# Performance work log

Hardware: AMD Instinct MI355X
Metric: run time of the kernel (lower is better)

Reference implementation:

```python
import math
import jax, jax.numpy as jnp
import numpy as np

# ---- static hyperparams (match init_kwargs) ----
B, D, K, NC, F = 16384, 64, 128, 64, 256
TAU_MIN = 0.01
TAU_DENOM_MIN = 0.001
EPS = 0.001  # transport_eps


def setup_inputs() -> dict:
    key = jax.random.key(0)
    ks = jax.random.split(key, 8)
    # latent positions strictly inside the Poincare ball (norm < 0.9)
    z = jax.random.normal(ks[0], (B, D), jnp.float32)
    z = z / (jnp.linalg.norm(z, axis=-1, keepdims=True) + 1e-6)
    z = z * (0.9 * jax.random.uniform(ks[1], (B, 1), jnp.float32))
    features = jax.random.normal(ks[2], (B, F), jnp.float32)
    q_z_w = jax.random.normal(ks[3], (K, D), jnp.float32) * 0.02
    q_z_b = jnp.zeros((K,), jnp.float32)
    q_feat_w = jax.random.normal(ks[4], (K, F), jnp.float32) * 0.02
    q_feat_b = jnp.zeros((K,), jnp.float32)
    q_gamma = jax.random.normal(ks[5], (K, D, D), jnp.float32) * 0.02
    chart_queries = jax.random.normal(ks[6], (NC, K), jnp.float32) * 0.02
    return {"z": z, "features": features, "q_z_w": q_z_w, "q_z_b": q_z_b,
            "q_feat_w": q_feat_w, "q_feat_b": q_feat_b, "q_gamma": q_gamma,
            "chart_queries": chart_queries}


def _hyperbolic_score(z, centers):
    # z: [B, D]; centers: [NC, D] -> scores [B, NC]
    diff = z[:, None, :] - centers[None, :, :]
    dist_sq = (diff ** 2).sum(-1)                       # [B, NC]
    z_sq = (z ** 2).sum(-1, keepdims=True)              # [B, 1]
    c_sq = (centers ** 2).sum(-1)[None, :]              # [1, NC]
    denom = (1.0 - z_sq) * (1.0 - c_sq)
    arg = 1.0 + 2.0 * dist_sq / (denom + EPS)
    dist = jnp.arccosh(jnp.maximum(arg, 1.0 + EPS))
    # metric-aware temperature tau(z)
    tau = math.sqrt(K) * jnp.maximum(1.0 - z_sq[:, 0], TAU_DENOM_MIN) / 2.0
    tau = jnp.maximum(tau, TAU_MIN)                     # [B]
    return -dist / tau[:, None]


def reference(z, features, q_z_w, q_z_b, q_feat_w, q_feat_b, q_gamma, chart_queries):
    # chart centers live in the first D coords of the chart queries
    centers = chart_queries[:, :D]                      # [NC, D]
    scores = _hyperbolic_score(z, centers)              # [B, NC]

    # query: linear(z) + linear(features) + bilinear gamma term
    q = z @ q_z_w.T + q_z_b + features @ q_feat_w.T + q_feat_b   # [B, K]
    q = q + jnp.einsum("bi,bj,kij->bk", z, z, q_gamma)           # gamma contraction

    # O(n) hyperbolic parallel transport: scale queries by 1/lambda(z)
    r2 = jnp.minimum((z ** 2).sum(-1, keepdims=True), 1.0 - EPS)  # [B, 1]
    lam = 2.0 / (1.0 - r2 + EPS)                                  # [B, 1]
    tq = chart_queries[None, :, :] / lam[:, None, :]              # [B, NC, K]

    scores = scores + jnp.einsum("bk,bnk->bn", q, tq) / math.sqrt(K)
    weights = jax.nn.softmax(scores, axis=-1)           # [B, NC] (soft routing)
    k_chart = jnp.argmax(weights, axis=-1)              # [B]
    return weights, k_chart
```

## Files before the change

### kernel.cpp

```cpp
#include <hip/hip_runtime.h>
#include <hip/hip_bf16.h>
#include <cmath>
#include <cstring>

#define B_TOT 16384

typedef unsigned int uint_t;
typedef unsigned short ushort_t;
typedef __attribute__((ext_vector_type(8))) short bf16x8;
typedef __attribute__((ext_vector_type(16))) float f32x16;

#define WS_TAB 0
#define WS_CSQ 1024
#define WS_LIN 4096
#define WS_S   4198400
#define WS_PPK 5246976

__global__ __launch_bounds__(256) void prep_s(const float* __restrict__ g,
                                              const float* __restrict__ cq,
                                              char* __restrict__ ws) {
  __shared__ float gl[128][68];
  __shared__ float cql[16][132];
  float* S = (float*)(ws + WS_S);
  const int ns = blockIdx.x >> 6, J = blockIdx.x & 63, t = threadIdx.x;
  for (int i = t; i < 2048; i += 256) {
    const int k = i >> 4, c4 = (i & 15) * 4;
    *(float4*)&gl[k][c4] = *(const float4*)(g + (size_t)k * 4096 + J * 64 + c4);
  }
  for (int i = t; i < 2048; i += 256) {
    const int n16 = i >> 7, k = i & 127;
    cql[n16][k] = cq[(ns * 16 + n16) * 128 + k];
  }
  __syncthreads();
  const int n16 = t >> 4, c4 = (t & 15) * 4;
  float4 acc = {0.f, 0.f, 0.f, 0.f};
#pragma unroll 8
  for (int k = 0; k < 128; ++k) {
    const float w = cql[n16][k];
    const float4 gv = *(const float4*)&gl[k][c4];
    acc.x = fmaf(w, gv.x, acc.x);
    acc.y = fmaf(w, gv.y, acc.y);
    acc.z = fmaf(w, gv.z, acc.z);
    acc.w = fmaf(w, gv.w, acc.w);
  }
  *(float4*)(S + (size_t)(ns * 16 + n16) * 4096 + J * 64 + c4) = acc;
}

__global__ __launch_bounds__(256) void prep_pack(
    const float* __restrict__ qfw, const float* __restrict__ cq,
    const float* __restrict__ qzw, const float* __restrict__ qzb,
    const float* __restrict__ qfb, char* __restrict__ ws) {
  __shared__ float Sl[4096];
  __shared__ uint_t tabl[192];
  __shared__ float psumf[128][2];
  const int n = blockIdx.x & 63, part = blockIdx.x >> 6, t = threadIdx.x;
  const float* __restrict__ S = (const float*)(ws + WS_S) + (size_t)n * 4096;
  for (int i = t; i < 4096; i += 256) Sl[i] = S[i];
  if (t < 64) {
    const int i = t;
    const int start = (i < 16) ? 4 * i
                     : (i < 32) ? 64 + 3 * (i - 16)
                     : (i < 48) ? 112 + 2 * (i - 32)
                                : 144 + (i - 48);
    const int nst = 4 - (i >> 4);
    for (int u = 0; u < nst; ++u)
      tabl[start + u] = (0u << 16) | ((uint_t)i << 8) | (uint_t)(16 * ((i >> 4) + u));
  } else if (t < 80) tabl[160 + (t - 64)] = (1u << 16) | (uint_t)((t - 64) * 16);
  else if (t < 84)   tabl[176 + (t - 80)] = (2u << 16) | (uint_t)((t - 80) * 16);
  else if (t == 84)  tabl[180] = (3u << 16);
  else if (t < 96)   tabl[181 + (t - 85)] = 0;
  __syncthreads();
  if (part == 0 && n == 0 && t < 192) ((uint_t*)(ws + WS_TAB))[t] = tabl[t];

  const int mt = n >> 5, r = n & 31;
  auto wpack = [&](int s, int jo, float val) {
    const __hip_bfloat16 hb = __float2bfloat16(val);
    const float hf = __bfloat162float(hb);
    const __hip_bfloat16 lb = __float2bfloat16(val - hf);
    ushort_t hu, lu;
    memcpy(&hu, &hb, 2);
    memcpy(&lu, &lb, 2);
    const size_t base =
        (((size_t)s * 4 + mt * 2) * 64 + ((jo >> 3) & 1) * 32 + r) * 16 + (jo & 7) * 2;
    *(ushort_t*)(ws + WS_PPK + base) = hu;
    *(ushort_t*)(ws + WS_PPK + base + 1024) = lu;
  };

  for (int v = part * 640 + t; v < (part + 1) * 640; v += 256) {
    const int s = v >> 4, jo = v & 15;
    const uint_t inf = tabl[s];
    const int i = (inf >> 8) & 255, j0 = inf & 255;
    const int j = j0 + jo;
    const float val =
        (j < i) ? 0.f : ((j > i) ? Sl[i * 64 + j] + Sl[j * 64 + i] : Sl[i * 64 + i]);
    wpack(s, jo, val);
  }
  const float* __restrict__ cqn = cq + n * 128;

  if (part >= 2) {
    const int fl = t & 127, kh = t >> 7;
    const int f = (part - 2) * 128 + fl;
    float a = 0.f;
#pragma unroll 8
    for (int k = 0; k < 64; ++k)
      a = fmaf(qfw[(kh * 64 + k) * 256 + f], cqn[kh * 64 + k], a);
    psumf[fl][kh] = a;
    __syncthreads();
    if (t < 128) {
      const int ff = (part - 2) * 128 + t;
      wpack(160 + (ff >> 4), ff & 15, psumf[t][0] + psumf[t][1]);
    }
  } else if (part == 1) {
    if (t < 64) {
      float a = 0.f;
#pragma unroll 8
      for (int k = 0; k < 128; ++k) a = fmaf(cqn[k], qzw[k * 64 + t], a);
      wpack(176 + (t >> 4), t & 15, a);
    }
    for (int v2 = t; v2 < 176; v2 += 256) wpack(181 + (v2 >> 4), v2 & 15, 0.f);
  } else {
    if (t == 128) {
      float a = 0.f;
      for (int k = 0; k < 128; ++k) a = fmaf(qzb[k] + qfb[k], cqn[k], a);
      wpack(180, 0, a);
    } else if (t > 128 && t < 144) wpack(180, t - 128, 0.f);
    if (t == 144) {
      double a = 0.0;
      for (int d = 0; d < 64; ++d) a = fma((double)cqn[d], (double)cqn[d], a);
      ((double*)(ws + WS_CSQ))[n] = a;
    }
  }
}

__global__ __launch_bounds__(256, 4) void gemm_tail_kernel(
    const float* __restrict__ z, const float* __restrict__ feat,
    const float* __restrict__ cq, char* __restrict__ ws,
    float* __restrict__ out) {
  __shared__ __align__(16) unsigned char smem[46208];
  float (*z_lds)[68] = (float (*)[68])(smem);
  float (*s_lin)[65] = (float (*)[65])(smem + 8704);
  float (*zt)[33] = (float (*)[33])(smem + 17024);
  float (*cqT)[65] = (float (*)[65])(smem + 25472);
  double (*s_exp)[65] = (double (*)[65])(smem + 25472);
  double (*pmax)[9] = (double (*)[9])(smem + 42112);
  int (*parg)[9] = (int (*)[9])(smem + 44416);
  double* rowmax = (double*)(smem + 45568);
  int* rowarg = (int*)(smem + 45824);
  double* rowinv = (double*)(smem + 45952);

  const int t = threadIdx.x, lane = t & 63;
  const int wv = __builtin_amdgcn_readfirstlane(t >> 6);
  const int b0 = blockIdx.x * 32;
  const int h = lane >> 5, c = lane & 31;

  for (int i = t; i < 2048; i += 256) z_lds[i >> 6][i & 63] = z[(size_t)b0 * 64 + i];
  if (t < 128) z_lds[t >> 2][64 + (t & 3)] = 0.f;
  for (int i = t; i < 32 * 65; i += 256) ((float*)s_lin)[i] = 0.f;
  __syncthreads();

  const bf16x8* __restrict__ pp = (const bf16x8*)(ws + WS_PPK);
  f32x16 acc[2] = {};
#pragma unroll 2
  for (int it = 0; it < 46; ++it) {
    const int s = wv + it * 4;
    int mode, i_idx, p0;
    if (s < 64) {
      mode = 0; i_idx = s >> 2; p0 = (s & 3) * 16;
    } else if (s < 112) {
      const int q = s - 64, d = (q * 86) >> 8;
      mode = 0; i_idx = 16 + d; p0 = (q - 3 * d + 1) * 16;
    } else if (s < 144) {
      const int q = s - 112;
      mode = 0; i_idx = 32 + (q >> 1); p0 = ((q & 1) + 2) * 16;
    } else if (s < 160) {
      mode = 0; i_idx = s - 96; p0 = 48;
    } else if (s < 176) {
      mode = 1; i_idx = 0; p0 = (s - 160) * 16;
    } else if (s < 180) {
      mode = 2; i_idx = 0; p0 = (s - 176) * 16;
    } else {
      mode = 3; i_idx = 0; p0 = 0;
    }
    const bf16x8 Ah0 = pp[((size_t)s * 4 + 0) * 64 + lane];
    const bf16x8 Al0 = pp[((size_t)s * 4 + 1) * 64 + lane];
    const bf16x8 Ah1 = pp[((size_t)s * 4 + 2) * 64 + lane];
    const bf16x8 Al1 = pp[((size_t)s * 4 + 3) * 64 + lane];
    const int bl = c;
    float xv[8];
    if (mode == 0) {
      const float zi = z_lds[bl][i_idx];
      const float* __restrict__ zp = &z_lds[bl][p0 + h * 8];
      const float4 a = *(const float4*)zp, b2 = *(const float4*)(zp + 4);
      xv[0] = zi * a.x; xv[1] = zi * a.y; xv[2] = zi * a.z; xv[3] = zi * a.w;
      xv[4] = zi * b2.x; xv[5] = zi * b2.y; xv[6] = zi * b2.z; xv[7] = zi * b2.w;
    } else if (mode == 1) {
      const float* __restrict__ fp = feat + (size_t)(b0 + bl) * 256 + p0 + h * 8;
      const float4 a = *(const float4*)fp, b2 = *(const float4*)(fp + 4);
      xv[0] = a.x; xv[1] = a.y; xv[2] = a.z; xv[3] = a.w;
      xv[4] = b2.x; xv[5] = b2.y; xv[6] = b2.z; xv[7] = b2.w;
    } else if (mode == 2) {
      const float* __restrict__ zp = &z_lds[bl][p0 + h * 8];
      const float4 a = *(const float4*)zp, b2 = *(const float4*)(zp + 4);
      xv[0] = a.x; xv[1] = a.y; xv[2] = a.z; xv[3] = a.w;
      xv[4] = b2.x; xv[5] = b2.y; xv[6] = b2.z; xv[7] = b2.w;
    } else {
      xv[0] = (h == 0) ? 1.f : 0.f;
      xv[1] = xv[2] = xv[3] = xv[4] = xv[5] = xv[6] = xv[7] = 0.f;
    }
    uint_t bhw[4], blw[4];
#pragma unroll
    for (int e2 = 0; e2 < 4; ++e2) {
      const float2 xp = {xv[2 * e2], xv[2 * e2 + 1]};
      const __hip_bfloat162 hb2 = __float22bfloat162_rn(xp);
      uint_t hw;
      memcpy(&hw, &hb2, 4);
      const float h0 = __uint_as_float(hw << 16);
      const float h1 = __uint_as_float(hw & 0xffff0000u);
      const float2 lp = {xp.x - h0, xp.y - h1};
      const __hip_bfloat162 lb2 = __float22bfloat162_rn(lp);
      uint_t lw;
      memcpy(&lw, &lb2, 4);
      bhw[e2] = hw;
      blw[e2] = lw;
    }
    bf16x8 Bh, Bl;
    memcpy(&Bh, bhw, 16);
    memcpy(&Bl, blw, 16);
    acc[0] = __builtin_amdgcn_mfma_f32_32x32x16_bf16(Ah0, Bh, acc[0], 0, 0, 0);
    acc[0] = __builtin_amdgcn_mfma_f32_32x32x16_bf16(Ah0, Bl, acc[0], 0, 0, 0);
    acc[0] = __builtin_amdgcn_mfma_f32_32x32x16_bf16(Al0, Bh, acc[0], 0, 0, 0);
    acc[1] = __builtin_amdgcn_mfma_f32_32x32x16_bf16(Ah1, Bh, acc[1], 0, 0, 0);
    acc[1] = __builtin_amdgcn_mfma_f32_32x32x16_bf16(Ah1, Bl, acc[1], 0, 0, 0);
    acc[1] = __builtin_amdgcn_mfma_f32_32x32x16_bf16(Al1, Bh, acc[1], 0, 0, 0);
  }
#pragma unroll
  for (int mt = 0; mt < 2; ++mt)
#pragma unroll
    for (int r = 0; r < 16; ++r) {
      const int n = mt * 32 + (r & 3) + 8 * (r >> 2) + 4 * h;
      atomicAdd(&s_lin[c][n], acc[mt][r]);
    }

  for (int i = t; i < 2048; i += 256) zt[i & 63][i >> 6] = z[(size_t)b0 * 64 + i];
  for (int i = t; i < 4096; i += 256) {
    const int n = i >> 6, ii = i & 63;
    cqT[ii][n] = cq[n * 128 + ii];
  }
  __syncthreads();

  const int r = t & 31, cg = t >> 5;

  double z_sq = 0.0, zc[8] = {0.0, 0.0, 0.0, 0.0, 0.0, 0.0, 0.0, 0.0};
#pragma unroll 4
  for (int i = 0; i < 64; ++i) {
    const double zv = (double)zt[i][r];
    z_sq = fma(zv, zv, z_sq);
#pragma unroll
    for (int u = 0; u < 8; ++u)
      zc[u] = fma(zv, (double)cqT[i][cg + 8 * u], zc[u]);
  }
  float lin[8];
#pragma unroll
  for (int u = 0; u < 8; ++u) lin[u] = s_lin[r][cg + 8 * u];

  const double EPS = 0.001;
  const double SQRTK = sqrt(128.0);
  double tau = SQRTK * fmax(1.0 - z_sq, 0.001) * 0.5;
  tau = fmax(tau, 0.01);
  const double inv_tau = 1.0 / tau;
  const double r2 = fmin(z_sq, 1.0 - EPS);
  const double lam_fac = (1.0 - r2 + EPS) * 0.5 / SQRTK;
  const double* __restrict__ csqd = (const double*)(ws + WS_CSQ);

  double sc[8];
#pragma unroll
  for (int u = 0; u < 8; ++u) {
    const int n = cg + 8 * u;
    const double c_sq = csqd[n];
    const double dist_sq = z_sq + c_sq - 2.0 * zc[u];
    const double denom = (1.0 - z_sq) * (1.0 - c_sq);
    float df = 2.0f * (float)dist_sq / ((float)denom + 0.001f);
    df = fmaxf(df, 0.001f);
    const float root = sqrtf(df * (df + 2.0f));
    const float dist = log1pf(df + root);
    sc[u] = -(double)dist * inv_tau + (double)lin[u] * lam_fac;
  }
  __syncthreads();

  {
    double mx = sc[0];
    int am = cg;
#pragma unroll
    for (int u = 1; u < 8; ++u)
      if (sc[u] > mx) { mx = sc[u]; am = cg + 8 * u; }
    pmax[r][cg] = mx;
    parg[r][cg] = am;
  }
  __syncthreads();
  if (t < 32) {
    double m = pmax[t][0];
    int a = parg[t][0];
#pragma unroll
    for (int g = 1; g < 8; ++g) {
      const double v = pmax[t][g];
      const int aa = parg[t][g];
      if (v > m || (v == m && aa < a)) { m = v; a = aa; }
    }
    rowmax[t] = m;
    rowarg[t] = a;
  }
  __syncthreads();
  {
    const double m = rowmax[r];
    double ps = 0.0;
#pragma unroll
    for (int u = 0; u < 8; ++u) {
      const double e = (double)expf((float)(sc[u] - m));
      s_exp[r][cg + 8 * u] = e;
      ps += e;
    }
    pmax[r][cg] = ps;
  }
  __syncthreads();
  if (t < 32) {
    double s = 0.0;
#pragma unroll
    for (int g = 0; g < 8; ++g) s += pmax[t][g];
    rowinv[t] = 1.0 / s;
  }
  __syncthreads();
  for (int idx = t; idx < 2048; idx += 256) {
    const int b = idx >> 6, n = idx & 63;
    out[(size_t)(b0 + b) * 64 + n] = (float)(s_exp[b][n] * rowinv[b]);
  }
  if (t < 32) out[(size_t)B_TOT * 64 + b0 + t] = (float)rowarg[t];
}

extern "C" void kernel_launch(void* const* d_in, const int* in_sizes, int n_in,
                              void* d_out, int out_size, void* d_ws, size_t ws_size,
                              hipStream_t stream) {
  const float* z = (const float*)d_in[0];
  const float* feat = (const float*)d_in[1];
  const float* qzw = (const float*)d_in[2];
  const float* qzb = (const float*)d_in[3];
  const float* qfw = (const float*)d_in[4];
  const float* qfb = (const float*)d_in[5];
  const float* gamma = (const float*)d_in[6];
  const float* cq = (const float*)d_in[7];
  float* out = (float*)d_out;
  char* ws = (char*)d_ws;

  prep_s<<<dim3(256), dim3(256), 0, stream>>>(gamma, cq, ws);
  prep_pack<<<dim3(256), dim3(256), 0, stream>>>(qfw, cq, qzw, qzb, qfb, ws);
  gemm_tail_kernel<<<dim3(B_TOT / 32), dim3(256), 0, stream>>>(z, feat, cq, ws, out);
}
```

Baseline: 155.6 us.

## Double-buffer packed weight chunks into LDS with async global-to-LDS loads

Each iteration's packed bf16 weight fragments are now prefetched one iteration ahead into a double-buffered LDS region with global_load_lds, instead of being loaded straight from global memory into registers. The goal is to hide global-load latency behind the MFMA work. The shared-memory layout is reshuffled and grown to hold the two 16 KB buffers. The cost is a workgroup barrier plus an explicit vmcnt wait every iteration. There is no reuse across waves, because each wave reads only its own slice. The overwrite of the previous buffer can also race with a slower wave that has not finished reading it.

```diff
diff --git a/kernel.cpp b/kernel.cpp
--- a/kernel.cpp
+++ b/kernel.cpp
@@ -136,17 +136,17 @@
     const float* __restrict__ z, const float* __restrict__ feat,
     const float* __restrict__ cq, char* __restrict__ ws,
     float* __restrict__ out) {
-  __shared__ __align__(16) unsigned char smem[46208];
-  float (*z_lds)[68] = (float (*)[68])(smem);
-  float (*s_lin)[65] = (float (*)[65])(smem + 8704);
-  float (*zt)[33] = (float (*)[33])(smem + 17024);
-  float (*cqT)[65] = (float (*)[65])(smem + 25472);
-  double (*s_exp)[65] = (double (*)[65])(smem + 25472);
-  double (*pmax)[9] = (double (*)[9])(smem + 42112);
-  int (*parg)[9] = (int (*)[9])(smem + 44416);
-  double* rowmax = (double*)(smem + 45568);
-  int* rowarg = (int*)(smem + 45824);
-  double* rowinv = (double*)(smem + 45952);
+  __shared__ __align__(16) unsigned char smem[49792];
+  float (*z_lds)[68] = (float (*)[68])(smem + 32768);
+  float (*s_lin)[65] = (float (*)[65])(smem + 41472);
+  float (*zt)[33] = (float (*)[33])(smem);
+  float (*cqT)[65] = (float (*)[65])(smem + 8448);
+  double (*s_exp)[65] = (double (*)[65])(smem + 8448);
+  double (*pmax)[9] = (double (*)[9])(smem + 25088);
+  int (*parg)[9] = (int (*)[9])(smem + 27392);
+  double* rowmax = (double*)(smem + 28544);
+  int* rowarg = (int*)(smem + 28800);
+  double* rowinv = (double*)(smem + 28928);
 
   const int t = threadIdx.x, lane = t & 63;
   const int wv = __builtin_amdgcn_readfirstlane(t >> 6);
@@ -156,13 +156,33 @@
   for (int i = t; i < 2048; i += 256) z_lds[i >> 6][i & 63] = z[(size_t)b0 * 64 + i];
   if (t < 128) z_lds[t >> 2][64 + (t & 3)] = 0.f;
   for (int i = t; i < 32 * 65; i += 256) ((float*)s_lin)[i] = 0.f;
-  __syncthreads();
-
-  const bf16x8* __restrict__ pp = (const bf16x8*)(ws + WS_PPK);
+
+  auto stage_chunk = [&](int cc, int buf) {
+    const char* gsrc = ws + WS_PPK + (size_t)cc * 16384 + (size_t)t * 16;
+    unsigned char* lb = smem + buf * 16384 + wv * 1024;
+#pragma unroll
+    for (int k = 0; k < 4; ++k)
+      __builtin_amdgcn_global_load_lds(
+          (const __attribute__((address_space(1))) void*)(gsrc + k * 4096),
+          (__attribute__((address_space(3))) void*)(lb + k * 4096), 16, 0, 0);
+  };
+
+  stage_chunk(0, 0);
+  __syncthreads();
+
   f32x16 acc[2] = {};
 #pragma unroll 2
   for (int it = 0; it < 46; ++it) {
-    const int s = wv + it * 4;
+    const int s = it * 4 + wv;
+    const int buf = it & 1;
+    if (it < 45) {
+      stage_chunk(it + 1, buf ^ 1);
+      asm volatile("s_waitcnt vmcnt(4)" ::: "memory");
+    } else {
+      asm volatile("s_waitcnt vmcnt(0)" ::: "memory");
+    }
+    __builtin_amdgcn_s_barrier();
+
     int mode, i_idx, p0;
     if (s < 64) {
       mode = 0; i_idx = s >> 2; p0 = (s & 3) * 16;
@@ -181,10 +201,12 @@
     } else {
       mode = 3; i_idx = 0; p0 = 0;
     }
-    const bf16x8 Ah0 = pp[((size_t)s * 4 + 0) * 64 + lane];
-    const bf16x8 Al0 = pp[((size_t)s * 4 + 1) * 64 + lane];
-    const bf16x8 Ah1 = pp[((size_t)s * 4 + 2) * 64 + lane];
-    const bf16x8 Al1 = pp[((size_t)s * 4 + 3) * 64 + lane];
+    const bf16x8* __restrict__ sp =
+        (const bf16x8*)(smem + buf * 16384 + wv * 4096);
+    const bf16x8 Ah0 = sp[lane];
+    const bf16x8 Al0 = sp[64 + lane];
+    const bf16x8 Ah1 = sp[128 + lane];
+    const bf16x8 Al1 = sp[192 + lane];
     const int bl = c;
     float xv[8];
     if (mode == 0) {
```

New measurement: 156.0 us. About the same (+0.3%).
